# Performance work log

Hardware: AMD Instinct MI355X
Metric: run time of the kernel (lower is better)

The kernel has to match this reference:

```python
import jax, jax.numpy as jnp
import numpy as np

B, C = 1, 1
D = H = W = 96
PD = PH = PW = 48
S = 24
ND = (D - PD) // S + 1          # 3 per axis
N = ND ** 3                     # 27 patches
ITEM = 2
EPS = 1e-8

def _lin_idx():
    d = (np.arange(ND) * S)[:, None] + np.arange(PD)      # [nd, pd] voxel coords per axis
    Dg = d[:, None, None, :, None, None]
    Hg = d[None, :, None, None, :, None]
    Wg = d[None, None, :, None, None, :]
    lin = (Dg * H + Hg) * W + Wg                           # [nd,nh,nw,pd,ph,pw]
    return lin.reshape(N, PD * PH * PW).astype(np.int32)

LIN = _lin_idx()
CNT = np.zeros(D * H * W, np.float32)
np.add.at(CNT, LIN.ravel(), 1.0)
CNT = np.maximum(CNT, 1e-6)                                # overlap weight (clamp_min 1e-6)

def extract(x):
    # [B,C,D,H,W] -> [N,B,C,pd,ph,pw] (as_strided overlap patches)
    p = x.reshape(B, C, D * H * W)[:, :, LIN]              # [B,C,N,ppp]
    return p.reshape(B, C, N, PD, PH, PW).transpose(2, 0, 1, 3, 4, 5)

def reconstruct(pat):
    # [N,B,C,pd,ph,pw] -> [B,C,D,H,W] overlap-add, divided by counts
    flat = pat.transpose(1, 2, 0, 3, 4, 5).reshape(B, C, N * PD * PH * PW)
    acc = jnp.zeros((B, C, D * H * W), pat.dtype).at[:, :, LIN.ravel()].add(flat)
    return (acc / CNT).reshape(B, C, D, H, W)

def conv3(x, w, b):
    y = jax.lax.conv_general_dilated(x, w, (1, 1, 1), [(1, 1)] * 3,
                                     dimension_numbers=('NCDHW', 'OIDHW', 'NCDHW'))
    return y + b.reshape(1, -1, 1, 1, 1)

def _forward(x, b, A, W1, b1, W2, b2):
    x_pat = extract(x)          # [N,B,C,pd,ph,pw]
    b_pat = extract(b)

    def gs_step(cur, inp):
        Ai, bi, i = inp                                         # Ai:[N,B,C,p...], bi:[B,C,p...]
        cross = jnp.einsum('n...,n...->...', Ai, cur)           # sum_j A[i,j]*x_j (mixed new/old)
        Aii = jnp.take(Ai, i, axis=0)
        coupling = cross - Aii * jnp.take(cur, i, axis=0)       # exclude j == i
        x_new = (bi - coupling) / (jax.nn.softplus(Aii) + EPS)
        return jax.lax.dynamic_update_index_in_dim(cur, x_new, i, 0), None

    xs = (A, b_pat, jnp.arange(N))
    x_last = x
    for _ in range(ITEM):
        cur, _ = jax.lax.scan(gs_step, x_pat, xs)               # Gauss-Seidel sweep
        x_last = reconstruct(cur)
        x_last = conv3(jax.nn.relu(conv3(x_last, W1, b1)), W2, b2)
        x_pat = extract(x_last)
    return x_last

def setup_inputs() -> dict:
    key = jax.random.key(0)
    k = jax.random.split(key, 5)
    A = jax.random.normal(k[2], (N, N, B, C, PD, PH, PW), jnp.float32) * 0.02
    A = 0.5 * (A + jnp.swapaxes(A, 0, 1))                       # A[i][j] == A[j][i] as in source
    return {
        'x': jax.random.normal(k[0], (B, C, D, H, W), jnp.float32),
        'b': jax.random.normal(k[1], (B, C, D, H, W), jnp.float32),
        'A': A,
        'W1': jax.random.normal(k[3], (16, 1, 3, 3, 3), jnp.float32) * 0.1,
        'b1': jnp.zeros((16,), jnp.float32),
        'W2': jax.random.normal(k[4], (1, 16, 3, 3, 3), jnp.float32) * 0.05,
        'b2': jnp.zeros((1,), jnp.float32),
    }

def reference(x, b, A, W1, b1, W2, b2):
    return _forward(x, b, A, W1, b1, W2, b2)
```

## Files before the change

### kernel.cpp

```cpp
#include <hip/hip_runtime.h>
#include <math.h>

#define NPAT 27
#define PATCH 110592
#define VOL 884736
#define GSBLK 128

#define XT 12
#define YT 10
#define YW 11

__device__ __forceinline__ float softplusf(float a) {
    return fmaxf(a, 0.f) + log1pf(expf(-fabsf(a)));
}

__global__ __launch_bounds__(GSBLK) void gs_sweep(
    const float* __restrict__ xf, const float* __restrict__ bg,
    const float* __restrict__ A, float* __restrict__ cur_out)
{
    __shared__ float cur[NPAT * GSBLK];
    const int tid = threadIdx.x;
    const int p = blockIdx.x * GSBLK + tid;
    const int pd = p / 2304;
    const int r0 = p - pd * 2304;
    const int ph = r0 / 48;
    const int pw = r0 - ph * 48;
    const int gbase = (pd * 96 + ph) * 96 + pw;

#pragma unroll
    for (int n = 0; n < NPAT; ++n) {
        const int nd = n / 9, nh = (n / 3) % 3, nw = n % 3;
        const int g = gbase + ((nd * 24) * 96 + nh * 24) * 96 + nw * 24;
        cur[n * GSBLK + tid] = xf[g];
    }

    const float* Ap = A + p;
#pragma unroll 1
    for (int i = 0; i < NPAT; ++i) {
        const float* Ai = Ap + (size_t)i * (NPAT * PATCH);
        float cross = 0.f;
#pragma unroll
        for (int n = 0; n < NPAT; ++n) {
            cross += __builtin_nontemporal_load(&Ai[(size_t)n * PATCH]) *
                     cur[n * GSBLK + tid];
        }
        const float aii = Ai[(size_t)i * PATCH];
        const float xi = cur[i * GSBLK + tid];
        const int id = i / 9, ih = (i / 3) % 3, iw = i % 3;
        const int g = gbase + ((id * 24) * 96 + ih * 24) * 96 + iw * 24;
        const float bi = bg[g];
        const float coupling = cross - aii * xi;
        const float xnew = (bi - coupling) / (softplusf(aii) + 1e-8f);
        cur[i * GSBLK + tid] = xnew;
    }

#pragma unroll
    for (int n = 0; n < NPAT; ++n) {
        cur_out[(size_t)n * PATCH + p] = cur[n * GSBLK + tid];
    }
}

__global__ __launch_bounds__(256) void fused_conv(
    const float* __restrict__ curp,
    const float* __restrict__ w1, const float* __restrict__ b1,
    const float* __restrict__ w2, const float* __restrict__ b2,
    float* __restrict__ out)
{
    __shared__ float xs[XT * XT * XT];
    __shared__ float ys[16 * YT * YT * YW];
    const int tid = threadIdx.x;
    const int bw = blockIdx.x % 12;
    const int bh = (blockIdx.x / 12) % 12;
    const int bd = blockIdx.x / 144;
    const int d0 = bd * 8, h0 = bh * 8, w0 = bw * 8;

    for (int l = tid; l < XT * XT * XT; l += 256) {
        const int ld = l / (XT * XT);
        const int r = l - ld * XT * XT;
        const int lh = r / XT, lw = r - lh * XT;
        const int gd = d0 + ld - 2, gh = h0 + lh - 2, gw = w0 + lw - 2;
        float v = 0.f;
        if ((unsigned)gd < 96u && (unsigned)gh < 96u && (unsigned)gw < 96u) {
            const int dlo = max(0, gd / 24 - 1), dhi = min(2, gd / 24);
            const int hlo = max(0, gh / 24 - 1), hhi = min(2, gh / 24);
            const int wlo = max(0, gw / 24 - 1), whi = min(2, gw / 24);
            float sum = 0.f;
            for (int nd = dlo; nd <= dhi; ++nd)
                for (int nh = hlo; nh <= hhi; ++nh)
                    for (int nw = wlo; nw <= whi; ++nw) {
                        const int n = nd * 9 + nh * 3 + nw;
                        const int pp = (gd - 24 * nd) * 2304 +
                                       (gh - 24 * nh) * 48 + (gw - 24 * nw);
                        sum += curp[(size_t)n * PATCH + pp];
                    }
            const int cnt = (dhi - dlo + 1) * (hhi - hlo + 1) * (whi - wlo + 1);
            v = sum / (float)cnt;
        }
        xs[l] = v;
    }
    __syncthreads();

    if (tid < 200) {
        const int sd = tid / 20;
        const int rr = tid - sd * 20;
        const int sh = rr >> 1;
        const int sw0 = (rr & 1) * 5;
        float xv[63];
#pragma unroll
        for (int kd = 0; kd < 3; ++kd)
#pragma unroll
            for (int kh = 0; kh < 3; ++kh)
#pragma unroll
                for (int j = 0; j < 7; ++j)
                    xv[(kd * 3 + kh) * 7 + j] =
                        xs[((sd + kd) * XT + (sh + kh)) * XT + sw0 + j];
        const int gdq = d0 + sd - 1, ghq = h0 + sh - 1;
        const bool okdh = ((unsigned)gdq < 96u) && ((unsigned)ghq < 96u);
        float msk[5];
#pragma unroll
        for (int j = 0; j < 5; ++j)
            msk[j] = (okdh && (unsigned)(w0 + sw0 + j - 1) < 96u) ? 1.f : 0.f;

#pragma unroll 1
        for (int c = 0; c < 16; ++c) {
            float wr[27];
#pragma unroll
            for (int k = 0; k < 27; ++k) wr[k] = w1[c * 27 + k];
            const float bb = b1[c];
            float acc[5] = {bb, bb, bb, bb, bb};
#pragma unroll
            for (int kd = 0; kd < 3; ++kd)
#pragma unroll
                for (int kh = 0; kh < 3; ++kh)
#pragma unroll
                    for (int kw = 0; kw < 3; ++kw) {
                        const float wgt = wr[kd * 9 + kh * 3 + kw];
                        const float* xvr = &xv[(kd * 3 + kh) * 7 + kw];
#pragma unroll
                        for (int j = 0; j < 5; ++j)
                            acc[j] += wgt * xvr[j];
                    }
            float* yrow = &ys[((c * YT + sd) * YT + sh) * YW + sw0];
#pragma unroll
            for (int j = 0; j < 5; ++j)
                yrow[j] = fmaxf(acc[j], 0.f) * msk[j];
        }
    }
    __syncthreads();

    if (tid < 128) {
        const int ow0 = (tid & 1) * 4;
        const int oh = (tid >> 1) & 7;
        const int od = tid >> 4;
        const float bb = b2[0];
        float a0 = bb, a1 = bb, a2 = bb, a3 = bb;
#pragma unroll 1
        for (int c = 0; c < 16; ++c) {
            float wr[27];
#pragma unroll
            for (int k = 0; k < 27; ++k) wr[k] = w2[c * 27 + k];
#pragma unroll
            for (int kd = 0; kd < 3; ++kd)
#pragma unroll
                for (int kh = 0; kh < 3; ++kh) {
                    const float* rowp =
                        &ys[((c * YT + od + kd) * YT + (oh + kh)) * YW + ow0];
                    const float v0 = rowp[0], v1 = rowp[1], v2 = rowp[2];
                    const float v3 = rowp[3], v4 = rowp[4], v5 = rowp[5];
                    const float wa = wr[kd * 9 + kh * 3 + 0];
                    const float wb = wr[kd * 9 + kh * 3 + 1];
                    const float wc = wr[kd * 9 + kh * 3 + 2];
                    a0 += wa * v0 + wb * v1 + wc * v2;
                    a1 += wa * v1 + wb * v2 + wc * v3;
                    a2 += wa * v2 + wb * v3 + wc * v4;
                    a3 += wa * v3 + wb * v4 + wc * v5;
                }
        }
        const int gd = d0 + od, gh = h0 + oh, gw = w0 + ow0;
        *(float4*)&out[(gd * 96 + gh) * 96 + gw] = make_float4(a0, a1, a2, a3);
    }
}

extern "C" void kernel_launch(void* const* d_in, const int* in_sizes, int n_in,
                              void* d_out, int out_size, void* d_ws, size_t ws_size,
                              hipStream_t stream)
{
    const float* x  = (const float*)d_in[0];
    const float* b  = (const float*)d_in[1];
    const float* A  = (const float*)d_in[2];
    const float* W1 = (const float*)d_in[3];
    const float* b1 = (const float*)d_in[4];
    const float* W2 = (const float*)d_in[5];
    const float* b2 = (const float*)d_in[6];
    float* out = (float*)d_out;

    float* cur  = (float*)d_ws;
    float* xnxt = cur + (size_t)NPAT * PATCH;

    const int gsGrid = PATCH / GSBLK;
    const int fGrid  = 12 * 12 * 12;

    gs_sweep<<<gsGrid, GSBLK, 0, stream>>>(x, b, A, cur);
    fused_conv<<<fGrid, 256, 0, stream>>>(cur, W1, b1, W2, b2, xnxt);
    gs_sweep<<<gsGrid, GSBLK, 0, stream>>>(xnxt, b, A, cur);
    fused_conv<<<fGrid, 256, 0, stream>>>(cur, W1, b1, W2, b2, out);
}
```

Baseline: 676.5 us.

## Register-resident GS sweep with A row prefetch; split conv channels into groups

The Gauss-Seidel kernel now keeps the 27 patch values in registers instead of shared memory. It fully unrolls the sweep and double-buffers the next row of A (27 loads) plus the next b value, so memory loads overlap the current row's dot product. The block size grows to 256. The fused conv processes its 16 hidden channels in two groups of 8, halving the shared-memory intermediate buffer to raise occupancy, at the cost of extra barriers. The register pressure from about 54 prefetched values plus 27 state values may limit occupancy or cause spills.

```diff
diff --git a/kernel.cpp b/kernel.cpp
--- a/kernel.cpp
+++ b/kernel.cpp
@@ -4,60 +4,68 @@
 #define NPAT 27
 #define PATCH 110592
 #define VOL 884736
-#define GSBLK 128
 
 #define XT 12
 #define YT 10
 #define YW 11
+#define CGRP 8
 
 __device__ __forceinline__ float softplusf(float a) {
     return fmaxf(a, 0.f) + log1pf(expf(-fabsf(a)));
 }
 
-__global__ __launch_bounds__(GSBLK) void gs_sweep(
+__global__ __launch_bounds__(256) void gs_sweep(
     const float* __restrict__ xf, const float* __restrict__ bg,
     const float* __restrict__ A, float* __restrict__ cur_out)
 {
-    __shared__ float cur[NPAT * GSBLK];
-    const int tid = threadIdx.x;
-    const int p = blockIdx.x * GSBLK + tid;
+    const int p = blockIdx.x * 256 + threadIdx.x;
     const int pd = p / 2304;
     const int r0 = p - pd * 2304;
     const int ph = r0 / 48;
     const int pw = r0 - ph * 48;
     const int gbase = (pd * 96 + ph) * 96 + pw;
 
+    float cur[NPAT];
 #pragma unroll
     for (int n = 0; n < NPAT; ++n) {
         const int nd = n / 9, nh = (n / 3) % 3, nw = n % 3;
-        const int g = gbase + ((nd * 24) * 96 + nh * 24) * 96 + nw * 24;
-        cur[n * GSBLK + tid] = xf[g];
+        cur[n] = xf[gbase + nd * 221184 + nh * 2304 + nw * 24];
     }
 
     const float* Ap = A + p;
-#pragma unroll 1
+    float a_cur[NPAT], a_nxt[NPAT];
+#pragma unroll
+    for (int n = 0; n < NPAT; ++n)
+        a_cur[n] = __builtin_nontemporal_load(&Ap[(size_t)n * PATCH]);
+    float b_cur = bg[gbase];
+    float b_nxt = 0.f;
+
+#pragma unroll
     for (int i = 0; i < NPAT; ++i) {
-        const float* Ai = Ap + (size_t)i * (NPAT * PATCH);
+        if (i + 1 < NPAT) {
+            const float* An = Ap + (size_t)(i + 1) * (NPAT * PATCH);
+#pragma unroll
+            for (int n = 0; n < NPAT; ++n)
+                a_nxt[n] = __builtin_nontemporal_load(&An[(size_t)n * PATCH]);
+            const int jd = (i + 1) / 9, jh = ((i + 1) / 3) % 3, jw = (i + 1) % 3;
+            b_nxt = bg[gbase + jd * 221184 + jh * 2304 + jw * 24];
+        }
         float cross = 0.f;
 #pragma unroll
-        for (int n = 0; n < NPAT; ++n) {
-            cross += __builtin_nontemporal_load(&Ai[(size_t)n * PATCH]) *
-                     cur[n * GSBLK + tid];
-        }
-        const float aii = Ai[(size_t)i * PATCH];
-        const float xi = cur[i * GSBLK + tid];
-        const int id = i / 9, ih = (i / 3) % 3, iw = i % 3;
-        const int g = gbase + ((id * 24) * 96 + ih * 24) * 96 + iw * 24;
-        const float bi = bg[g];
-        const float coupling = cross - aii * xi;
-        const float xnew = (bi - coupling) / (softplusf(aii) + 1e-8f);
-        cur[i * GSBLK + tid] = xnew;
-    }
-
-#pragma unroll
-    for (int n = 0; n < NPAT; ++n) {
-        cur_out[(size_t)n * PATCH + p] = cur[n * GSBLK + tid];
-    }
+        for (int n = 0; n < NPAT; ++n)
+            cross += a_cur[n] * cur[n];
+        const float aii = a_cur[i];
+        const float coupling = cross - aii * cur[i];
+        cur[i] = (b_cur - coupling) / (softplusf(aii) + 1e-8f);
+#pragma unroll
+        for (int n = 0; n < NPAT; ++n)
+            a_cur[n] = a_nxt[n];
+        b_cur = b_nxt;
+    }
+
+#pragma unroll
+    for (int n = 0; n < NPAT; ++n)
+        cur_out[(size_t)n * PATCH + p] = cur[n];
 }
 
 __global__ __launch_bounds__(256) void fused_conv(
@@ -67,7 +75,7 @@
     float* __restrict__ out)
 {
     __shared__ float xs[XT * XT * XT];
-    __shared__ float ys[16 * YT * YT * YW];
+    __shared__ float ys[CGRP * YT * YT * YW];
     const int tid = threadIdx.x;
     const int bw = blockIdx.x % 12;
     const int bh = (blockIdx.x / 12) % 12;
@@ -98,14 +106,29 @@
         }
         xs[l] = v;
     }
+
+    const int sd = tid / 20;
+    const int rr = tid - sd * 20;
+    const int sh = rr >> 1;
+    const int sw0 = (rr & 1) * 5;
+    const int ow0 = (tid & 1) * 4;
+    const int oh = (tid >> 1) & 7;
+    const int od = tid >> 4;
+
+    const float bb2 = b2[0];
+    float a0 = bb2, a1 = bb2, a2 = bb2, a3 = bb2;
+
+    float xv[63];
+    float msk[5];
+    if (tid < 200) {
+        const int gdq = d0 + sd - 1, ghq = h0 + sh - 1;
+        const bool okdh = ((unsigned)gdq < 96u) && ((unsigned)ghq < 96u);
+#pragma unroll
+        for (int j = 0; j < 5; ++j)
+            msk[j] = (okdh && (unsigned)(w0 + sw0 + j - 1) < 96u) ? 1.f : 0.f;
+    }
     __syncthreads();
-
     if (tid < 200) {
-        const int sd = tid / 20;
-        const int rr = tid - sd * 20;
-        const int sh = rr >> 1;
-        const int sw0 = (rr & 1) * 5;
-        float xv[63];
 #pragma unroll
         for (int kd = 0; kd < 3; ++kd)
 #pragma unroll
@@ -114,68 +137,68 @@
                 for (int j = 0; j < 7; ++j)
                     xv[(kd * 3 + kh) * 7 + j] =
                         xs[((sd + kd) * XT + (sh + kh)) * XT + sw0 + j];
-        const int gdq = d0 + sd - 1, ghq = h0 + sh - 1;
-        const bool okdh = ((unsigned)gdq < 96u) && ((unsigned)ghq < 96u);
-        float msk[5];
-#pragma unroll
-        for (int j = 0; j < 5; ++j)
-            msk[j] = (okdh && (unsigned)(w0 + sw0 + j - 1) < 96u) ? 1.f : 0.f;
+    }
 
 #pragma unroll 1
-        for (int c = 0; c < 16; ++c) {
-            float wr[27];
-#pragma unroll
-            for (int k = 0; k < 27; ++k) wr[k] = w1[c * 27 + k];
-            const float bb = b1[c];
-            float acc[5] = {bb, bb, bb, bb, bb};
-#pragma unroll
-            for (int kd = 0; kd < 3; ++kd)
-#pragma unroll
-                for (int kh = 0; kh < 3; ++kh)
-#pragma unroll
-                    for (int kw = 0; kw < 3; ++kw) {
-                        const float wgt = wr[kd * 9 + kh * 3 + kw];
-                        const float* xvr = &xv[(kd * 3 + kh) * 7 + kw];
-#pragma unroll
-                        for (int j = 0; j < 5; ++j)
-                            acc[j] += wgt * xvr[j];
+    for (int grp = 0; grp < 2; ++grp) {
+        if (tid < 200) {
+#pragma unroll 1
+            for (int cc = 0; cc < CGRP; ++cc) {
+                const int c = grp * CGRP + cc;
+                float wr[27];
+#pragma unroll
+                for (int k = 0; k < 27; ++k) wr[k] = w1[c * 27 + k];
+                const float bb = b1[c];
+                float acc[5] = {bb, bb, bb, bb, bb};
+#pragma unroll
+                for (int kd = 0; kd < 3; ++kd)
+#pragma unroll
+                    for (int kh = 0; kh < 3; ++kh)
+#pragma unroll
+                        for (int kw = 0; kw < 3; ++kw) {
+                            const float wgt = wr[kd * 9 + kh * 3 + kw];
+                            const float* xvr = &xv[(kd * 3 + kh) * 7 + kw];
+#pragma unroll
+                            for (int j = 0; j < 5; ++j)
+                                acc[j] += wgt * xvr[j];
+                        }
+                float* yrow = &ys[((cc * YT + sd) * YT + sh) * YW + sw0];
+#pragma unroll
+                for (int j = 0; j < 5; ++j)
+                    yrow[j] = fmaxf(acc[j], 0.f) * msk[j];
+            }
+        }
+        __syncthreads();
+
+        if (tid < 128) {
+#pragma unroll 1
+            for (int cc = 0; cc < CGRP; ++cc) {
+                const int c = grp * CGRP + cc;
+                float wr[27];
+#pragma unroll
+                for (int k = 0; k < 27; ++k) wr[k] = w2[c * 27 + k];
+#pragma unroll
+                for (int kd = 0; kd < 3; ++kd)
+#pragma unroll
+                    for (int kh = 0; kh < 3; ++kh) {
+                        const float* rowp =
+                            &ys[((cc * YT + od + kd) * YT + (oh + kh)) * YW + ow0];
+                        const float v0 = rowp[0], v1 = rowp[1], v2 = rowp[2];
+                        const float v3 = rowp[3], v4 = rowp[4], v5 = rowp[5];
+                        const float wa = wr[kd * 9 + kh * 3 + 0];
+                        const float wb = wr[kd * 9 + kh * 3 + 1];
+                        const float wc = wr[kd * 9 + kh * 3 + 2];
+                        a0 += wa * v0 + wb * v1 + wc * v2;
+                        a1 += wa * v1 + wb * v2 + wc * v3;
+                        a2 += wa * v2 + wb * v3 + wc * v4;
+                        a3 += wa * v3 + wb * v4 + wc * v5;
                     }
-            float* yrow = &ys[((c * YT + sd) * YT + sh) * YW + sw0];
-#pragma unroll
-            for (int j = 0; j < 5; ++j)
-                yrow[j] = fmaxf(acc[j], 0.f) * msk[j];
-        }
-    }
-    __syncthreads();
+            }
+        }
+        __syncthreads();
+    }
 
     if (tid < 128) {
-        const int ow0 = (tid & 1) * 4;
-        const int oh = (tid >> 1) & 7;
-        const int od = tid >> 4;
-        const float bb = b2[0];
-        float a0 = bb, a1 = bb, a2 = bb, a3 = bb;
-#pragma unroll 1
-        for (int c = 0; c < 16; ++c) {
-            float wr[27];
-#pragma unroll
-            for (int k = 0; k < 27; ++k) wr[k] = w2[c * 27 + k];
-#pragma unroll
-            for (int kd = 0; kd < 3; ++kd)
-#pragma unroll
-                for (int kh = 0; kh < 3; ++kh) {
-                    const float* rowp =
-                        &ys[((c * YT + od + kd) * YT + (oh + kh)) * YW + ow0];
-                    const float v0 = rowp[0], v1 = rowp[1], v2 = rowp[2];
-                    const float v3 = rowp[3], v4 = rowp[4], v5 = rowp[5];
-                    const float wa = wr[kd * 9 + kh * 3 + 0];
-                    const float wb = wr[kd * 9 + kh * 3 + 1];
-                    const float wc = wr[kd * 9 + kh * 3 + 2];
-                    a0 += wa * v0 + wb * v1 + wc * v2;
-                    a1 += wa * v1 + wb * v2 + wc * v3;
-                    a2 += wa * v2 + wb * v3 + wc * v4;
-                    a3 += wa * v3 + wb * v4 + wc * v5;
-                }
-        }
         const int gd = d0 + od, gh = h0 + oh, gw = w0 + ow0;
         *(float4*)&out[(gd * 96 + gh) * 96 + gw] = make_float4(a0, a1, a2, a3);
     }
@@ -197,11 +220,11 @@
     float* cur  = (float*)d_ws;
     float* xnxt = cur + (size_t)NPAT * PATCH;
 
-    const int gsGrid = PATCH / GSBLK;
+    const int gsGrid = PATCH / 256;
     const int fGrid  = 12 * 12 * 12;
 
-    gs_sweep<<<gsGrid, GSBLK, 0, stream>>>(x, b, A, cur);
+    gs_sweep<<<gsGrid, 256, 0, stream>>>(x, b, A, cur);
     fused_conv<<<fGrid, 256, 0, stream>>>(cur, W1, b1, W2, b2, xnxt);
-    gs_sweep<<<gsGrid, GSBLK, 0, stream>>>(xnxt, b, A, cur);
+    gs_sweep<<<gsGrid, 256, 0, stream>>>(xnxt, b, A, cur);
     fused_conv<<<fGrid, 256, 0, stream>>>(cur, W1, b1, W2, b2, out);
 }
```

Result: no change. 682.1 us (+0.8%).
